# Kernel tuning notes

Hardware: AMD Instinct MI355X
Metric: run time of the kernel (lower is better)

## Reference

```python
import jax, jax.numpy as jnp
import numpy as np

B, M, N = 1, 128, 256          # batch, MSA rows, residues
C_IN, C_PAIR = 256, 128        # rep1d_feat, rep2d_feat
H, C = 8, 32                   # num_heads, attention_num_c
EPS = 1e-5


def layer_norm(x, g, b):
    mu = jnp.mean(x, axis=-1, keepdims=True)
    var = jnp.var(x, axis=-1, keepdims=True)
    return (x - mu) * jax.lax.rsqrt(var + EPS) * g + b


def setup_inputs() -> dict:
    key = jax.random.key(0)
    ks = jax.random.split(key, 10)
    s_in = 1.0 / np.sqrt(C_IN)
    s_pair = 1.0 / np.sqrt(C_PAIR)
    s_hc = 1.0 / np.sqrt(H * C)
    return {
        "x1d": jax.random.normal(ks[0], (B, M, N, C_IN), jnp.float32),
        "x2d": jax.random.normal(ks[1], (B, N, N, C_PAIR), jnp.float32),
        "ln1_g": jnp.ones((C_IN,), jnp.float32),
        "ln1_b": jnp.zeros((C_IN,), jnp.float32),
        "ln2_g": jnp.ones((C_PAIR,), jnp.float32),
        "ln2_b": jnp.zeros((C_PAIR,), jnp.float32),
        "Wq": jax.random.normal(ks[2], (C_IN, H * C), jnp.float32) * s_in,
        "Wk": jax.random.normal(ks[3], (C_IN, H * C), jnp.float32) * s_in,
        "Wv": jax.random.normal(ks[4], (C_IN, H * C), jnp.float32) * s_in,
        "W2d": jax.random.normal(ks[5], (C_PAIR, H), jnp.float32) * s_pair,
        "Wgate": jax.random.normal(ks[6], (C_IN, H * C), jnp.float32) * s_in,
        "bgate": jnp.zeros((H * C,), jnp.float32),
        "Wfinal": jax.random.normal(ks[7], (H * C, C_IN), jnp.float32) * s_hc,
        "bfinal": jnp.zeros((C_IN,), jnp.float32),
    }


def reference(x1d, x2d, ln1_g, ln1_b, ln2_g, ln2_b,
              Wq, Wk, Wv, W2d, Wgate, bgate, Wfinal, bfinal):
    x1 = layer_norm(x1d, ln1_g, ln1_b)                      # [b,m,i,c_in]
    x2 = layer_norm(x2d, ln2_g, ln2_b)                      # [b,i,j,c_pair]
    bias = jnp.einsum('bijp,ph->bhij', x2, W2d)             # [b,h,i,j]

    factor = 1.0 / np.sqrt(C).astype(np.float32)
    q = jnp.einsum('bmid,dhc->bmihc', x1, Wq.reshape(C_IN, H, C)) * factor
    k = jnp.einsum('bmid,dhc->bmihc', x1, Wk.reshape(C_IN, H, C))
    v = jnp.einsum('bmid,dhc->bmihc', x1, Wv.reshape(C_IN, H, C))

    aff = jnp.einsum('bmihc,bmjhc->bmhij', q, k)            # [b,m,h,i,j]
    weights = jax.nn.softmax(aff + bias[:, None], axis=-1)

    gate = jax.nn.sigmoid(
        jnp.einsum('bmid,dhc->bmihc', x1, Wgate.reshape(C_IN, H, C))
        + bgate.reshape(1, 1, 1, H, C))

    out = jnp.einsum('bmhqk,bmkhc->bmqhc', weights, v) * gate
    out = jnp.einsum('bmqhc,hcd->bmqd', out, Wfinal.reshape(H, C, C_IN)) + bfinal
    return out
```

## Files before the change

kernel.cpp:

```cpp
#include <hip/hip_runtime.h>


typedef unsigned short u16;
typedef unsigned int   u32;
typedef __attribute__((ext_vector_type(8))) __bf16 bf16x8;
typedef __attribute__((ext_vector_type(4))) float  f32x4;

#define DEV __device__ __forceinline__

DEV float bf2f(u16 s) {
    u32 u = ((u32)s) << 16;
    float f;
    __builtin_memcpy(&f, &u, 4);
    return f;
}
DEV u16 f2bf(float f) {
    u32 u;
    __builtin_memcpy(&u, &f, 4);
    u = (u + 0x7fffu + ((u >> 16) & 1u)) >> 16;
    return (u16)u;
}

__global__ void k_transpose(const float* __restrict__ Wq, const float* __restrict__ Wk,
                            const float* __restrict__ Wv, const float* __restrict__ Wg,
                            const float* __restrict__ Wf,
                            u16* __restrict__ WT, u16* __restrict__ WfT) {
    int idx = blockIdx.x * 256 + threadIdx.x;
    if (idx < 1024 * 256) {
        int gcol = idx >> 8, p = idx & 255;
        int sel = gcol >> 8, c = gcol & 255;
        const float* W = sel == 0 ? Wq : sel == 1 ? Wk : sel == 2 ? Wv : Wg;
        WT[idx] = f2bf(W[p * 256 + c]);
    } else {
        int j = idx - 1024 * 256;
        int d = j >> 8, hc = j & 255;
        WfT[j] = f2bf(Wf[hc * 256 + d]);
    }
}

__global__ __launch_bounds__(256) void k_ln1(const float* __restrict__ x,
                                             const float* __restrict__ gg,
                                             const float* __restrict__ bb,
                                             u16* __restrict__ y) {
    int lane = threadIdx.x & 63, wave = threadIdx.x >> 6;
    int row = blockIdx.x * 4 + wave;
    float4 xv = *(const float4*)(x + row * 256 + lane * 4);
    float v0 = xv.x, v1 = xv.y, v2 = xv.z, v3 = xv.w;
    float s  = v0 + v1 + v2 + v3;
    float s2 = v0*v0 + v1*v1 + v2*v2 + v3*v3;
    #pragma unroll
    for (int msk = 32; msk; msk >>= 1) {
        s  += __shfl_xor(s,  msk, 64);
        s2 += __shfl_xor(s2, msk, 64);
    }
    float mu  = s * (1.0f / 256.0f);
    float var = s2 * (1.0f / 256.0f) - mu * mu;
    float rs  = rsqrtf(var + 1e-5f);
    float4 gv = *(const float4*)(gg + lane * 4);
    float4 bv = *(const float4*)(bb + lane * 4);
    ushort4 o;
    o.x = f2bf((v0 - mu) * rs * gv.x + bv.x);
    o.y = f2bf((v1 - mu) * rs * gv.y + bv.y);
    o.z = f2bf((v2 - mu) * rs * gv.z + bv.z);
    o.w = f2bf((v3 - mu) * rs * gv.w + bv.w);
    *(ushort4*)(y + row * 256 + lane * 4) = o;
}

__global__ __launch_bounds__(256) void k_ln2bias(const float* __restrict__ x2,
                                                 const float* __restrict__ gg,
                                                 const float* __restrict__ bb,
                                                 const float* __restrict__ W2d,
                                                 float* __restrict__ bias) {
    int lane = threadIdx.x & 63, wave = threadIdx.x >> 6;
    int row = blockIdx.x * 4 + wave;
    float2 xv = *(const float2*)(x2 + row * 128 + lane * 2);
    float v0 = xv.x, v1 = xv.y;
    float s = v0 + v1, s2 = v0*v0 + v1*v1;
    #pragma unroll
    for (int msk = 32; msk; msk >>= 1) {
        s  += __shfl_xor(s,  msk, 64);
        s2 += __shfl_xor(s2, msk, 64);
    }
    float mu  = s * (1.0f / 128.0f);
    float var = s2 * (1.0f / 128.0f) - mu * mu;
    float rs  = rsqrtf(var + 1e-5f);
    float2 gv = *(const float2*)(gg + lane * 2);
    float2 bv = *(const float2*)(bb + lane * 2);
    float xn0 = (v0 - mu) * rs * gv.x + bv.x;
    float xn1 = (v1 - mu) * rs * gv.y + bv.y;
    int p0 = lane * 2;
    float4 w0a = *(const float4*)(W2d + p0 * 8);
    float4 w0b = *(const float4*)(W2d + p0 * 8 + 4);
    float4 w1a = *(const float4*)(W2d + (p0 + 1) * 8);
    float4 w1b = *(const float4*)(W2d + (p0 + 1) * 8 + 4);
    float p[8];
    p[0] = xn0 * w0a.x + xn1 * w1a.x;
    p[1] = xn0 * w0a.y + xn1 * w1a.y;
    p[2] = xn0 * w0a.z + xn1 * w1a.z;
    p[3] = xn0 * w0a.w + xn1 * w1a.w;
    p[4] = xn0 * w0b.x + xn1 * w1b.x;
    p[5] = xn0 * w0b.y + xn1 * w1b.y;
    p[6] = xn0 * w0b.z + xn1 * w1b.z;
    p[7] = xn0 * w0b.w + xn1 * w1b.w;
    #pragma unroll
    for (int hh = 0; hh < 8; hh++)
        #pragma unroll
        for (int msk = 32; msk; msk >>= 1)
            p[hh] += __shfl_xor(p[hh], msk, 64);
    if (lane == 0) {
        #pragma unroll
        for (int hh = 0; hh < 8; hh++)
            bias[hh * 65536 + row] = p[hh];
    }
}

DEV void mfma_tile64(const u16* __restrict__ X, const u16* __restrict__ WTb,
                     int rowbase, int colbase, int K, f32x4 acc[4][4], int lane) {
    int lrow = lane & 15, lk = (lane >> 4) * 8;
    for (int kk = 0; kk < K; kk += 32) {
        bf16x8 af[4], bf[4];
        #pragma unroll
        for (int t = 0; t < 4; t++)
            af[t] = *(const bf16x8*)(X + (rowbase + t * 16 + lrow) * K + kk + lk);
        #pragma unroll
        for (int t = 0; t < 4; t++)
            bf[t] = *(const bf16x8*)(WTb + (colbase + t * 16 + lrow) * K + kk + lk);
        #pragma unroll
        for (int i = 0; i < 4; i++)
            #pragma unroll
            for (int j = 0; j < 4; j++)
                acc[i][j] = __builtin_amdgcn_mfma_f32_16x16x32_bf16(af[i], bf[j], acc[i][j], 0, 0, 0);
    }
}

__global__ __launch_bounds__(256) void k_qkvg(const u16* __restrict__ X, const u16* __restrict__ WT,
                                              u16* __restrict__ q, u16* __restrict__ kb,
                                              u16* __restrict__ vt, u16* __restrict__ gt,
                                              const float* __restrict__ bgate) {
    int lane = threadIdx.x & 63, wave = threadIdx.x >> 6;
    int rowbase = blockIdx.x * 128 + (wave >> 1) * 64;
    int colbase = blockIdx.y * 128 + (wave & 1) * 64;
    f32x4 acc[4][4];
    #pragma unroll
    for (int i = 0; i < 4; i++)
        #pragma unroll
        for (int j = 0; j < 4; j++)
            acc[i][j] = (f32x4){0.f, 0.f, 0.f, 0.f};
    mfma_tile64(X, WT, rowbase, colbase, 256, acc, lane);
    int lrow = lane & 15, quad = lane >> 4;
    int which = blockIdx.y >> 1;
    #pragma unroll
    for (int it = 0; it < 4; it++)
        #pragma unroll
        for (int jt = 0; jt < 4; jt++)
            #pragma unroll
            for (int r = 0; r < 4; r++) {
                int grow = rowbase + it * 16 + quad * 4 + r;
                int gcol = colbase + jt * 16 + lrow;
                int o = gcol & 255;
                float v = acc[it][jt][r];
                if (which == 0) {
                    q[grow * 256 + o] = f2bf(v * 0.17677669529663687f);
                } else if (which == 1) {
                    kb[grow * 256 + o] = f2bf(v);
                } else if (which == 2) {
                    int mm = grow >> 8, ii = grow & 255;
                    vt[(mm * 256 + o) * 256 + ii] = f2bf(v);
                } else {
                    float z = v + bgate[o];
                    gt[grow * 256 + o] = f2bf(1.0f / (1.0f + __expf(-z)));
                }
            }
}

__global__ __launch_bounds__(256) void k_attn(const u16* __restrict__ q, const u16* __restrict__ kb,
                                              const u16* __restrict__ vt, const u16* __restrict__ gt,
                                              const float* __restrict__ bias,
                                              u16* __restrict__ tmp) {
    __shared__ u16 P[4][16][264];
    int lane = threadIdx.x & 63, wave = threadIdx.x >> 6;
    int lrow = lane & 15, quad = lane >> 4, lk = quad * 8;
    int m = blockIdx.x, h = blockIdx.y, iblk = blockIdx.z;
    int i0 = iblk * 64 + wave * 16;

    bf16x8 aq = *(const bf16x8*)(q + (m * 256 + i0 + lrow) * 256 + h * 32 + lk);
    f32x4 acc[16];
    #pragma unroll
    for (int jt = 0; jt < 16; jt++) {
        bf16x8 bk = *(const bf16x8*)(kb + (m * 256 + jt * 16 + lrow) * 256 + h * 32 + lk);
        f32x4 z = {0.f, 0.f, 0.f, 0.f};
        acc[jt] = __builtin_amdgcn_mfma_f32_16x16x32_bf16(aq, bk, z, 0, 0, 0);
    }

    float rmax[4] = {-1e30f, -1e30f, -1e30f, -1e30f};
    #pragma unroll
    for (int jt = 0; jt < 16; jt++)
        #pragma unroll
        for (int r = 0; r < 4; r++) {
            int i = i0 + quad * 4 + r;
            int j = jt * 16 + lrow;
            float a = acc[jt][r] + bias[h * 65536 + i * 256 + j];
            acc[jt][r] = a;
            rmax[r] = fmaxf(rmax[r], a);
        }
    #pragma unroll
    for (int r = 0; r < 4; r++)
        #pragma unroll
        for (int msk = 8; msk; msk >>= 1)
            rmax[r] = fmaxf(rmax[r], __shfl_xor(rmax[r], msk, 64));
    float rsum[4] = {0.f, 0.f, 0.f, 0.f};
    #pragma unroll
    for (int jt = 0; jt < 16; jt++)
        #pragma unroll
        for (int r = 0; r < 4; r++) {
            float e = __expf(acc[jt][r] - rmax[r]);
            acc[jt][r] = e;
            rsum[r] += e;
        }
    #pragma unroll
    for (int r = 0; r < 4; r++) {
        #pragma unroll
        for (int msk = 8; msk; msk >>= 1)
            rsum[r] += __shfl_xor(rsum[r], msk, 64);
        rsum[r] = 1.0f / fmaxf(rsum[r], 1e-30f);
    }

    #pragma unroll
    for (int jt = 0; jt < 16; jt++)
        #pragma unroll
        for (int r = 0; r < 4; r++)
            P[wave][quad * 4 + r][jt * 16 + lrow] = f2bf(acc[jt][r] * rsum[r]);
    __syncthreads();

    f32x4 oacc[2] = {{0.f,0.f,0.f,0.f}, {0.f,0.f,0.f,0.f}};
    const u16* Pw = &P[wave][0][0];
    for (int kk2 = 0; kk2 < 256; kk2 += 32) {
        bf16x8 ap = *(const bf16x8*)(Pw + lrow * 264 + kk2 + lk);
        #pragma unroll
        for (int ct = 0; ct < 2; ct++) {
            bf16x8 bv = *(const bf16x8*)(vt + (m * 256 + h * 32 + ct * 16 + lrow) * 256 + kk2 + lk);
            oacc[ct] = __builtin_amdgcn_mfma_f32_16x16x32_bf16(ap, bv, oacc[ct], 0, 0, 0);
        }
    }

    #pragma unroll
    for (int ct = 0; ct < 2; ct++)
        #pragma unroll
        for (int r = 0; r < 4; r++) {
            int i = i0 + quad * 4 + r;
            int o = h * 32 + ct * 16 + lrow;
            float gv = bf2f(gt[(m * 256 + i) * 256 + o]);
            tmp[(m * 256 + i) * 256 + o] = f2bf(oacc[ct][r] * gv);
        }
}

__global__ __launch_bounds__(256) void k_final(const u16* __restrict__ T, const u16* __restrict__ WfT,
                                               const float* __restrict__ bfinal, float* __restrict__ out) {
    int lane = threadIdx.x & 63, wave = threadIdx.x >> 6;
    int rowbase = blockIdx.x * 128 + (wave >> 1) * 64;
    int colbase = blockIdx.y * 128 + (wave & 1) * 64;
    f32x4 acc[4][4];
    #pragma unroll
    for (int i = 0; i < 4; i++)
        #pragma unroll
        for (int j = 0; j < 4; j++)
            acc[i][j] = (f32x4){0.f, 0.f, 0.f, 0.f};
    mfma_tile64(T, WfT, rowbase, colbase, 256, acc, lane);
    int lrow = lane & 15, quad = lane >> 4;
    #pragma unroll
    for (int it = 0; it < 4; it++)
        #pragma unroll
        for (int jt = 0; jt < 4; jt++)
            #pragma unroll
            for (int r = 0; r < 4; r++) {
                int grow = rowbase + it * 16 + quad * 4 + r;
                int gcol = colbase + jt * 16 + lrow;
                out[grow * 256 + gcol] = acc[it][jt][r] + bfinal[gcol];
            }
}

extern "C" void kernel_launch(void* const* d_in, const int* in_sizes, int n_in,
                              void* d_out, int out_size, void* d_ws, size_t ws_size,
                              hipStream_t stream) {
    const float* x1d   = (const float*)d_in[0];
    const float* x2d   = (const float*)d_in[1];
    const float* ln1_g = (const float*)d_in[2];
    const float* ln1_b = (const float*)d_in[3];
    const float* ln2_g = (const float*)d_in[4];
    const float* ln2_b = (const float*)d_in[5];
    const float* Wq    = (const float*)d_in[6];
    const float* Wk    = (const float*)d_in[7];
    const float* Wv    = (const float*)d_in[8];
    const float* W2d   = (const float*)d_in[9];
    const float* Wg    = (const float*)d_in[10];
    const float* bg    = (const float*)d_in[11];
    const float* Wf    = (const float*)d_in[12];
    const float* bfin  = (const float*)d_in[13];
    float* out = (float*)d_out;

    char* ws = (char*)d_ws;
    u16*   x1   = (u16*)(ws);
    u16*   WT   = (u16*)(ws + 16777216);
    u16*   WfT  = (u16*)(ws + 17301504);
    float* bias = (float*)(ws + 17432576);
    u16*   qb   = (u16*)(ws + 19529728);
    u16*   kb   = (u16*)(ws + 36306944);
    u16*   vtb  = (u16*)(ws + 53084160);
    u16*   gb   = (u16*)(ws + 69861376);
    u16*   tmp  = x1;

    k_transpose<<<1280, 256, 0, stream>>>(Wq, Wk, Wv, Wg, Wf, WT, WfT);
    k_ln1<<<8192, 256, 0, stream>>>(x1d, ln1_g, ln1_b, x1);
    k_ln2bias<<<16384, 256, 0, stream>>>(x2d, ln2_g, ln2_b, W2d, bias);
    k_qkvg<<<dim3(256, 8), 256, 0, stream>>>(x1, WT, qb, kb, vtb, gb, bg);
    k_attn<<<dim3(128, 8, 4), 256, 0, stream>>>(qb, kb, vtb, gb, bias, tmp);
    k_final<<<dim3(256, 2), 256, 0, stream>>>(tmp, WfT, bfin, out);
}
```

Measured before the change: 358.6 us.

## Stage GEMM operand tiles in LDS via direct global-to-LDS loads with XOR swizzle

Replaces the per-wave direct-global-load MFMA GEMM core with a block-cooperative version. Each K=64 slice of the 128x128 A and B tiles is loaded into shared memory with global_load_lds, using an XOR swizzle to avoid bank conflicts, and the waves then read their fragments from LDS. The goal is to cut redundant global/L2 traffic, since waves sharing rows or columns previously fetched the same data separately. In exchange it adds 32KB of LDS per block and two barriers per K step with no double buffering, which may lower occupancy and expose load latency.

```diff
diff --git a/kernel.cpp b/kernel.cpp
--- a/kernel.cpp
+++ b/kernel.cpp
@@ -20,6 +20,11 @@
     u = (u + 0x7fffu + ((u >> 16) & 1u)) >> 16;
     return (u16)u;
 }
+
+#define GLD_LDS16(gp, lp)                                                           \
+    __builtin_amdgcn_global_load_lds(                                               \
+        (const __attribute__((address_space(1))) u32*)(const void*)(gp),            \
+        (__attribute__((address_space(3))) u32*)(void*)(lp), 16, 0, 0)
 
 __global__ void k_transpose(const float* __restrict__ Wq, const float* __restrict__ Wk,
                             const float* __restrict__ Wv, const float* __restrict__ Wg,
@@ -114,22 +119,49 @@
     }
 }
 
-DEV void mfma_tile64(const u16* __restrict__ X, const u16* __restrict__ WTb,
-                     int rowbase, int colbase, int K, f32x4 acc[4][4], int lane) {
-    int lrow = lane & 15, lk = (lane >> 4) * 8;
-    for (int kk = 0; kk < K; kk += 32) {
-        bf16x8 af[4], bf[4];
-        #pragma unroll
-        for (int t = 0; t < 4; t++)
-            af[t] = *(const bf16x8*)(X + (rowbase + t * 16 + lrow) * K + kk + lk);
-        #pragma unroll
-        for (int t = 0; t < 4; t++)
-            bf[t] = *(const bf16x8*)(WTb + (colbase + t * 16 + lrow) * K + kk + lk);
-        #pragma unroll
-        for (int i = 0; i < 4; i++)
-            #pragma unroll
-            for (int j = 0; j < 4; j++)
-                acc[i][j] = __builtin_amdgcn_mfma_f32_16x16x32_bf16(af[i], bf[j], acc[i][j], 0, 0, 0);
+DEV void gemm128_core(const u16* __restrict__ X, const u16* __restrict__ WTb,
+                      int rowbase, int colbase, int K,
+                      u16* As, u16* Bs, f32x4 acc[4][4], int lane, int wave) {
+    int l8 = lane & 7, r8 = lane >> 3;
+    int gchunk = l8 ^ (r8 & 7);
+    int lrow = lane & 15, quad = lane >> 4;
+    int wr = (wave >> 1) * 64, wc = (wave & 1) * 64;
+
+    for (int kk = 0; kk < K; kk += 64) {
+        #pragma unroll
+        for (int i = 0; i < 4; i++) {
+            int s = wave * 4 + i;
+            const u16* g = X + (rowbase + s * 8 + r8) * K + kk + gchunk * 8;
+            GLD_LDS16(g, As + s * 512);
+        }
+        #pragma unroll
+        for (int i = 0; i < 4; i++) {
+            int s = wave * 4 + i;
+            const u16* g = WTb + (colbase + s * 8 + r8) * K + kk + gchunk * 8;
+            GLD_LDS16(g, Bs + s * 512);
+        }
+        __syncthreads();
+        #pragma unroll
+        for (int k2 = 0; k2 < 64; k2 += 32) {
+            int cidx = (k2 >> 3) + quad;
+            bf16x8 af[4], bf[4];
+            #pragma unroll
+            for (int t = 0; t < 4; t++) {
+                int R = wr + t * 16 + lrow;
+                af[t] = *(const bf16x8*)(As + R * 64 + ((cidx ^ (R & 7)) << 3));
+            }
+            #pragma unroll
+            for (int t = 0; t < 4; t++) {
+                int R = wc + t * 16 + lrow;
+                bf[t] = *(const bf16x8*)(Bs + R * 64 + ((cidx ^ (R & 7)) << 3));
+            }
+            #pragma unroll
+            for (int i = 0; i < 4; i++)
+                #pragma unroll
+                for (int j = 0; j < 4; j++)
+                    acc[i][j] = __builtin_amdgcn_mfma_f32_16x16x32_bf16(af[i], bf[j], acc[i][j], 0, 0, 0);
+        }
+        __syncthreads();
     }
 }
 
@@ -137,17 +169,20 @@
                                               u16* __restrict__ q, u16* __restrict__ kb,
                                               u16* __restrict__ vt, u16* __restrict__ gt,
                                               const float* __restrict__ bgate) {
-    int lane = threadIdx.x & 63, wave = threadIdx.x >> 6;
-    int rowbase = blockIdx.x * 128 + (wave >> 1) * 64;
-    int colbase = blockIdx.y * 128 + (wave & 1) * 64;
+    __shared__ u16 As[128 * 64];
+    __shared__ u16 Bs[128 * 64];
+    int lane = threadIdx.x & 63, wave = threadIdx.x >> 6;
+    int rowbase = blockIdx.x * 128;
+    int colbase = blockIdx.y * 128;
     f32x4 acc[4][4];
     #pragma unroll
     for (int i = 0; i < 4; i++)
         #pragma unroll
         for (int j = 0; j < 4; j++)
             acc[i][j] = (f32x4){0.f, 0.f, 0.f, 0.f};
-    mfma_tile64(X, WT, rowbase, colbase, 256, acc, lane);
+    gemm128_core(X, WT, rowbase, colbase, 256, As, Bs, acc, lane, wave);
     int lrow = lane & 15, quad = lane >> 4;
+    int wrb = rowbase + (wave >> 1) * 64, wcb = colbase + (wave & 1) * 64;
     int which = blockIdx.y >> 1;
     #pragma unroll
     for (int it = 0; it < 4; it++)
@@ -155,8 +190,8 @@
         for (int jt = 0; jt < 4; jt++)
             #pragma unroll
             for (int r = 0; r < 4; r++) {
-                int grow = rowbase + it * 16 + quad * 4 + r;
-                int gcol = colbase + jt * 16 + lrow;
+                int grow = wrb + it * 16 + quad * 4 + r;
+                int gcol = wcb + jt * 16 + lrow;
                 int o = gcol & 255;
                 float v = acc[it][jt][r];
                 if (which == 0) {
@@ -256,25 +291,28 @@
 
 __global__ __launch_bounds__(256) void k_final(const u16* __restrict__ T, const u16* __restrict__ WfT,
                                                const float* __restrict__ bfinal, float* __restrict__ out) {
-    int lane = threadIdx.x & 63, wave = threadIdx.x >> 6;
-    int rowbase = blockIdx.x * 128 + (wave >> 1) * 64;
-    int colbase = blockIdx.y * 128 + (wave & 1) * 64;
+    __shared__ u16 As[128 * 64];
+    __shared__ u16 Bs[128 * 64];
+    int lane = threadIdx.x & 63, wave = threadIdx.x >> 6;
+    int rowbase = blockIdx.x * 128;
+    int colbase = blockIdx.y * 128;
     f32x4 acc[4][4];
     #pragma unroll
     for (int i = 0; i < 4; i++)
         #pragma unroll
         for (int j = 0; j < 4; j++)
             acc[i][j] = (f32x4){0.f, 0.f, 0.f, 0.f};
-    mfma_tile64(T, WfT, rowbase, colbase, 256, acc, lane);
+    gemm128_core(T, WfT, rowbase, colbase, 256, As, Bs, acc, lane, wave);
     int lrow = lane & 15, quad = lane >> 4;
+    int wrb = rowbase + (wave >> 1) * 64, wcb = colbase + (wave & 1) * 64;
     #pragma unroll
     for (int it = 0; it < 4; it++)
         #pragma unroll
         for (int jt = 0; jt < 4; jt++)
             #pragma unroll
             for (int r = 0; r < 4; r++) {
-                int grow = rowbase + it * 16 + quad * 4 + r;
-                int gcol = colbase + jt * 16 + lrow;
+                int grow = wrb + it * 16 + quad * 4 + r;
+                int gcol = wcb + jt * 16 + lrow;
                 out[grow * 256 + gcol] = acc[it][jt][r] + bfinal[gcol];
             }
 }
```

Result: faster. 312.8 us (-12.7%).
